# Performance work log

Measured on AMD Instinct MI355X. Metric: run time of the kernel, lower is better.

The kernel has to match this reference:

```python
import jax, jax.numpy as jnp
import numpy as np

N_NODES = 100000
N_EDGES = 1000000
N_GRAPHS = 64
NODE_IN = 4
HID = 64
SIG = 16
NEG_SLOPE = 0.2


def _gat_layer(x, src, dst, W, a_src, a_dst, bias, n_nodes, concat):
    # W: [H*D, F_in], a_src/a_dst: [H, D], bias: [H*D] or [D]
    H, D = a_src.shape
    h = (x @ W.T).reshape(-1, H, D)                      # [N, H, D]
    alpha_src = jnp.sum(h * a_src[None], axis=-1)        # [N, H]
    alpha_dst = jnp.sum(h * a_dst[None], axis=-1)        # [N, H]
    e = alpha_src[src] + alpha_dst[dst]                  # [E, H]
    e = jax.nn.leaky_relu(e, NEG_SLOPE)
    # segment softmax over edges grouped by destination node
    e_max = jax.ops.segment_max(e, dst, num_segments=n_nodes)   # [N, H]
    e_exp = jnp.exp(e - e_max[dst])                              # [E, H]
    denom = jax.ops.segment_sum(e_exp, dst, num_segments=n_nodes)
    alpha = e_exp / denom[dst]                                   # [E, H]
    out = jax.ops.segment_sum(alpha[:, :, None] * h[src], dst, num_segments=n_nodes)  # [N,H,D]
    if concat:
        out = out.reshape(-1, H * D)
    else:
        out = out.mean(axis=1)
    return out + bias


def setup_inputs() -> dict:
    key = jax.random.key(0)
    ks = jax.random.split(key, 16)
    x = jax.random.normal(ks[0], (N_NODES, NODE_IN), dtype=jnp.float32)
    edge_index = jax.random.randint(ks[1], (2, N_EDGES), 0, N_NODES, dtype=jnp.int32)
    batch = jnp.sort(jax.random.randint(ks[2], (N_NODES,), 0, N_GRAPHS, dtype=jnp.int32))
    s = 0.1
    # conv1: heads=2, concat -> out 128
    w1 = jax.random.normal(ks[3], (2 * HID, NODE_IN), dtype=jnp.float32) * s
    att_src1 = jax.random.normal(ks[4], (2, HID), dtype=jnp.float32) * s
    att_dst1 = jax.random.normal(ks[5], (2, HID), dtype=jnp.float32) * s
    b1 = jnp.zeros((2 * HID,), dtype=jnp.float32)
    # conv2: heads=1, mean -> out 64
    w2 = jax.random.normal(ks[6], (HID, 2 * HID), dtype=jnp.float32) * s
    att_src2 = jax.random.normal(ks[7], (1, HID), dtype=jnp.float32) * s
    att_dst2 = jax.random.normal(ks[8], (1, HID), dtype=jnp.float32) * s
    b2 = jnp.zeros((HID,), dtype=jnp.float32)
    wp = jax.random.normal(ks[9], (SIG, HID), dtype=jnp.float32) * s
    bp = jnp.zeros((SIG,), dtype=jnp.float32)
    return {"x": x, "edge_index": edge_index, "batch": batch,
            "w1": w1, "att_src1": att_src1, "att_dst1": att_dst1, "b1": b1,
            "w2": w2, "att_src2": att_src2, "att_dst2": att_dst2, "b2": b2,
            "wp": wp, "bp": bp}


def reference(x, edge_index, batch, w1, att_src1, att_dst1, b1,
              w2, att_src2, att_dst2, b2, wp, bp):
    n = x.shape[0]
    loops = jnp.arange(n, dtype=edge_index.dtype)
    src = jnp.concatenate([edge_index[0], loops])  # PyG GATConv adds self-loops
    dst = jnp.concatenate([edge_index[1], loops])
    h = jax.nn.elu(_gat_layer(x, src, dst, w1, att_src1, att_dst1, b1, n, concat=True))
    h = jax.nn.elu(_gat_layer(h, src, dst, w2, att_src2, att_dst2, b2, n, concat=False))
    # global mean pool by graph id
    sums = jax.ops.segment_sum(h, batch, num_segments=N_GRAPHS)
    cnts = jax.ops.segment_sum(jnp.ones((n,), h.dtype), batch, num_segments=N_GRAPHS)
    pooled = sums / jnp.maximum(cnts, 1.0)[:, None]
    return (pooled @ wp.T + bp).squeeze()
```

## Files before the change

kernel.cpp:

```cpp
#include <hip/hip_runtime.h>
#include <hip/hip_fp16.h>

#define N_NODES  100000
#define N_EDGES  1000000
#define E_TOT    1100000
#define E_CAP    1900000
#define N_GRAPHS 64

#define BSH    9
#define BSIZE  512
#define NBUCK  ((N_NODES + BSIZE - 1) / BSIZE)
#define CHUNK  4096
#define NBLKS  ((E_TOT + CHUNK - 1) / CHUNK)

typedef _Float16 half8 __attribute__((ext_vector_type(8)));
typedef float    f32x4 __attribute__((ext_vector_type(4)));

__device__ __forceinline__ float elu_f(float v) {
    return v > 0.f ? v : expm1f(v);
}

__device__ __forceinline__ float lrelu(float v) {
    return v > 0.f ? v : 0.2f * v;
}

__device__ __forceinline__ int lbound(const int* __restrict__ a, int n, int v) {
    int lo = 0, hi = n;
    while (lo < hi) { int m = (lo + hi) >> 1; if (a[m] < v) lo = m + 1; else hi = m; }
    return lo;
}

__global__ void k_preall(const float* __restrict__ w1,
                         const float* __restrict__ as1v, const float* __restrict__ ad1v,
                         const float* __restrict__ w2,
                         const float* __restrict__ as2v, const float* __restrict__ ad2v,
                         float* __restrict__ A1, float* __restrict__ D1,
                         float* __restrict__ B2, float* __restrict__ E2,
                         __half* __restrict__ w2frag,
                         int* __restrict__ bucketCount, float* __restrict__ pool,
                         const int* __restrict__ batch, float* __restrict__ cnt)
{
    if (blockIdx.x == 0) {
        int t = threadIdx.x;
        if (t < 128) {
            float acc = 0.f;
            for (int d = 0; d < 64; ++d) acc += w2[d * 128 + t] * as2v[d];
            B2[t] = acc;
        } else {
            int k = t - 128;
            float acc = 0.f;
            for (int d = 0; d < 64; ++d) acc += w2[d * 128 + k] * ad2v[d];
            E2[k] = acc;
        }
        if (t < 8) {
            int h = t >> 2, k = t & 3;
            float acc = 0.f;
            for (int d = 0; d < 64; ++d) acc += w1[(h * 64 + d) * 4 + k] * as1v[h * 64 + d];
            A1[t] = acc;
        } else if (t < 16) {
            int i = t - 8, h = i >> 2, k = i & 3;
            float acc = 0.f;
            for (int d = 0; d < 64; ++d) acc += w1[(h * 64 + d) * 4 + k] * ad1v[h * 64 + d];
            D1[i] = acc;
        }
        if (t < NBUCK) bucketCount[t] = 0;
        if (t < N_GRAPHS) {
            int a = lbound(batch, N_NODES, t);
            int b = lbound(batch, N_NODES, t + 1);
            cnt[t] = (float)(b - a);
        }
    } else {
        int f = (blockIdx.x - 1) * 256 + threadIdx.x;
        int j = f & 7, ln = (f >> 3) & 63, g = f >> 9;
        int nt = g >> 2, ks = g & 3;
        int col = nt * 16 + (ln & 15);
        int k   = ks * 32 + ((ln >> 4) << 3) + j;
        w2frag[f] = __float2half(w2[col * 128 + k]);
        if (f < N_GRAPHS * 64) pool[f] = 0.f;
    }
}

__global__ void __launch_bounds__(256) k_bin1(
    const int* __restrict__ ei, int* __restrict__ bucketCount, int* __restrict__ blockoff)
{
    __shared__ int hist[NBUCK];
    const int t = threadIdx.x;
    for (int i = t; i < NBUCK; i += 256) hist[i] = 0;
    __syncthreads();
    const int e0 = blockIdx.x * CHUNK;
    for (int i = t; i < CHUNK; i += 256) {
        int e = e0 + i;
        if (e < E_TOT) {
            int dst = (e < N_EDGES) ? ei[N_EDGES + e] : (e - N_EDGES);
            atomicAdd(&hist[dst >> BSH], 1);
        }
    }
    __syncthreads();
    for (int i = t; i < NBUCK; i += 256)
        blockoff[blockIdx.x * NBUCK + i] = atomicAdd(&bucketCount[i], hist[i]);
}

__global__ void __launch_bounds__(256) k_bin2(
    const int* __restrict__ ei, const int* __restrict__ bucketCount,
    const int* __restrict__ blockoff, int* __restrict__ bucketStart,
    unsigned int* __restrict__ bucketed)
{
    __shared__ int sh[256];
    __shared__ int cur[NBUCK];
    const int t = threadIdx.x;
    int v = (t < NBUCK) ? bucketCount[t] : 0;
    int acc = v;
    sh[t] = acc; __syncthreads();
    for (int off = 1; off < 256; off <<= 1) {
        int add = (t >= off) ? sh[t - off] : 0;
        __syncthreads();
        acc += add; sh[t] = acc; __syncthreads();
    }
    if (t < NBUCK) {
        int st = acc - v;
        cur[t] = st + blockoff[blockIdx.x * NBUCK + t];
        if (blockIdx.x == 0) bucketStart[t] = st;
    }
    __syncthreads();
    const int e0 = blockIdx.x * CHUNK;
    for (int i = t; i < CHUNK; i += 256) {
        int e = e0 + i;
        if (e < E_TOT) {
            int src = (e < N_EDGES) ? ei[e] : (e - N_EDGES);
            int dst = (e < N_EDGES) ? ei[N_EDGES + e] : (e - N_EDGES);
            int b = dst >> BSH;
            int p = atomicAdd(&cur[b], 1);
            bucketed[p] = (unsigned)src | ((unsigned)(dst & (BSIZE - 1)) << 17);
        }
    }
}

__global__ void __launch_bounds__(256) k_bhist(
    const unsigned int* __restrict__ bucketed,
    const int* __restrict__ bucketStart, const int* __restrict__ bucketCount,
    int* __restrict__ deg, int* __restrict__ rowptr, int* __restrict__ bucketPad)
{
    __shared__ int hist[BSIZE];
    __shared__ int sh[256];
    const int t = threadIdx.x;
    const int b = blockIdx.x;
    hist[t] = 0; hist[t + 256] = 0;
    __syncthreads();
    const int beg = bucketStart[b], cnt = bucketCount[b];
    for (int i = t; i < cnt; i += 256)
        atomicAdd(&hist[bucketed[beg + i] >> 17], 1);
    __syncthreads();
    int h0 = hist[2 * t], h1 = hist[2 * t + 1];
    int a = (h0 + 7) & ~7, c = (h1 + 7) & ~7;
    int s = a + c;
    sh[t] = s; __syncthreads();
    for (int off = 1; off < 256; off <<= 1) {
        int add = (t >= off) ? sh[t - off] : 0;
        __syncthreads();
        s += add; sh[t] = s; __syncthreads();
    }
    int base = s - a - c;
    const int n0 = b * BSIZE;
    int na = n0 + 2 * t, nb = n0 + 2 * t + 1;
    if (na < N_NODES) { deg[na] = h0; rowptr[na] = base; }
    if (nb < N_NODES) { deg[nb] = h1; rowptr[nb] = base + a; }
    if (t == 255) bucketPad[b] = s;
}

__global__ void __launch_bounds__(256) k_bscat(
    const unsigned int* __restrict__ bucketed,
    const int* __restrict__ bucketStart, const int* __restrict__ bucketCount,
    const int* __restrict__ bucketPad,
    int* __restrict__ rowptr, int* __restrict__ srcs)
{
    __shared__ int sh[256];
    __shared__ int excl[NBUCK];
    __shared__ int cur[BSIZE];
    const int t = threadIdx.x;
    const int b = blockIdx.x;

    int v = (t < NBUCK) ? bucketPad[t] : 0;
    int acc = v;
    sh[t] = acc; __syncthreads();
    for (int off = 1; off < 256; off <<= 1) {
        int add = (t >= off) ? sh[t - off] : 0;
        __syncthreads();
        acc += add; sh[t] = acc; __syncthreads();
    }
    if (t < NBUCK) excl[t] = acc - v;
    if (b == 0 && t == NBUCK - 1) rowptr[N_NODES] = acc;
    __syncthreads();
    const int base = excl[b];

    const int n0 = b * BSIZE;
    #pragma unroll
    for (int k = 0; k < 2; ++k) {
        int nl = t + k * 256;
        int n = n0 + nl;
        if (n < N_NODES) {
            int r = rowptr[n] + base;
            rowptr[n] = r;
            cur[nl] = r;
        }
    }
    __syncthreads();
    const int beg = bucketStart[b], cnt = bucketCount[b];
    for (int i = t; i < cnt; i += 256) {
        unsigned p = bucketed[beg + i];
        int rank = atomicAdd(&cur[p >> 17], 1);
        srcs[rank] = (int)(p & 0x1FFFFu);
    }
    __syncthreads();
    const int bend = base + bucketPad[b];
    #pragma unroll
    for (int k = 0; k < 2; ++k) {
        int nl = t + k * 256;
        int n = n0 + nl;
        if (n < N_NODES) {
            int e = (nl == BSIZE - 1 || n == N_NODES - 1) ? bend : rowptr[n + 1];
            for (int j = cur[nl]; j < e; ++j) srcs[j] = -1;
        }
    }
}

__global__ void __launch_bounds__(256) k_gather1x(
    const int* __restrict__ srcs, const int* __restrict__ rowptr, const int* __restrict__ deg,
    const float* __restrict__ x,
    const float* __restrict__ A1c, const float* __restrict__ D1c,
    float4* __restrict__ agg0, float4* __restrict__ agg1, float2* __restrict__ wsA)
{
    const int tid  = threadIdx.x;
    const int n    = blockIdx.x * 16 + (tid >> 4);
    const int lane = tid & 15;
    if (n >= N_NODES) return;

    const float4 A0 = ((const float4*)A1c)[0], A1v = ((const float4*)A1c)[1];
    const float4 D0 = ((const float4*)D1c)[0], D1v = ((const float4*)D1c)[1];
    const float4 xn = ((const float4*)x)[n];
    const float ad0 = xn.x * D0.x + xn.y * D0.y + xn.z * D0.z + xn.w * D0.w;
    const float ad1 = xn.x * D1v.x + xn.y * D1v.y + xn.z * D1v.z + xn.w * D1v.w;

    const int beg = rowptr[n], rend = beg + deg[n];
    float4 acc0 = {0.f, 0.f, 0.f, 0.f}, acc1 = {0.f, 0.f, 0.f, 0.f};
    float ws0 = 0.f, ws1 = 0.f;
    for (int j = beg + lane; j < rend; j += 16) {
        const int s = srcs[j];
        const float4 xs = ((const float4*)x)[s];
        const float as0 = xs.x * A0.x + xs.y * A0.y + xs.z * A0.z + xs.w * A0.w;
        const float as1 = xs.x * A1v.x + xs.y * A1v.y + xs.z * A1v.z + xs.w * A1v.w;
        const float w0 = __expf(lrelu(as0 + ad0));
        const float w1 = __expf(lrelu(as1 + ad1));
        acc0.x = fmaf(w0, xs.x, acc0.x); acc0.y = fmaf(w0, xs.y, acc0.y);
        acc0.z = fmaf(w0, xs.z, acc0.z); acc0.w = fmaf(w0, xs.w, acc0.w);
        acc1.x = fmaf(w1, xs.x, acc1.x); acc1.y = fmaf(w1, xs.y, acc1.y);
        acc1.z = fmaf(w1, xs.z, acc1.z); acc1.w = fmaf(w1, xs.w, acc1.w);
        ws0 += w0; ws1 += w1;
    }
    #pragma unroll
    for (int off = 1; off < 16; off <<= 1) {
        acc0.x += __shfl_xor(acc0.x, off, 64);
        acc0.y += __shfl_xor(acc0.y, off, 64);
        acc0.z += __shfl_xor(acc0.z, off, 64);
        acc0.w += __shfl_xor(acc0.w, off, 64);
        acc1.x += __shfl_xor(acc1.x, off, 64);
        acc1.y += __shfl_xor(acc1.y, off, 64);
        acc1.z += __shfl_xor(acc1.z, off, 64);
        acc1.w += __shfl_xor(acc1.w, off, 64);
        ws0    += __shfl_xor(ws0,    off, 64);
        ws1    += __shfl_xor(ws1,    off, 64);
    }
    if (lane == 0) {
        agg0[n] = acc0;
        agg1[n] = acc1;
        wsA[n]  = make_float2(ws0, ws1);
    }
}

#define H2_NPB 64
#define SROW_H_LD 136
__global__ void __launch_bounds__(256) k_h2f(
    const float4* __restrict__ agg0, const float4* __restrict__ agg1,
    const float2* __restrict__ wsA,
    const float* __restrict__ w1, const float* __restrict__ b1,
    const __half* __restrict__ w2frag,
    const float* __restrict__ B2, const float* __restrict__ E2,
    __half* __restrict__ h2h, float* __restrict__ as2, float* __restrict__ ad2)
{
    __shared__ __align__(16) _Float16 srow[H2_NPB * SROW_H_LD];
    const int tid = threadIdx.x;
    const int bn  = blockIdx.x * H2_NPB;

    #pragma unroll 4
    for (int t = 0; t < 16; ++t) {
        int i = tid + t * 256;
        int r = i >> 6, c2 = i & 63;
        int n = bn + r;
        int head = c2 >> 5;
        float4 a; float ws;
        if (n < N_NODES) {
            a = head ? agg1[n] : agg0[n];
            float2 w = wsA[n];
            ws = head ? w.y : w.x;
        } else { a = make_float4(0.f, 0.f, 0.f, 0.f); ws = 1.f; }
        const float4 wA = ((const float4*)w1)[2 * c2];
        const float4 wB = ((const float4*)w1)[2 * c2 + 1];
        const float2 bb = ((const float2*)b1)[c2];
        float inv = 1.f / ws;
        float v0 = elu_f((a.x * wA.x + a.y * wA.y + a.z * wA.z + a.w * wA.w) * inv + bb.x);
        float v1 = elu_f((a.x * wB.x + a.y * wB.y + a.z * wB.z + a.w * wB.w) * inv + bb.y);
        *(__half2*)&srow[r * SROW_H_LD + 2 * c2] = __floats2half2_rn(v0, v1);
    }
    __syncthreads();

    {
        int r = tid >> 2, q = tid & 3;
        const __half2* row = (const __half2*)&srow[r * SROW_H_LD];
        float ps = 0.f, pd = 0.f;
        #pragma unroll 4
        for (int i = 0; i < 16; ++i) {
            int c2 = q * 16 + i;
            float2 v  = __half22float2(row[c2]);
            float2 Bv = ((const float2*)B2)[c2];
            float2 Ev = ((const float2*)E2)[c2];
            ps += v.x * Bv.x + v.y * Bv.y;
            pd += v.x * Ev.x + v.y * Ev.y;
        }
        ps += __shfl_xor(ps, 1, 64); ps += __shfl_xor(ps, 2, 64);
        pd += __shfl_xor(pd, 1, 64); pd += __shfl_xor(pd, 2, 64);
        int n = bn + r;
        if (q == 0 && n < N_NODES) { as2[n] = ps; ad2[n] = pd; }
    }

    const int lane = tid & 63;
    const int wv   = tid >> 6;
    const int mrow = lane & 15;
    const int kc   = lane >> 4;
    f32x4 acc[4] = {{0.f,0.f,0.f,0.f},{0.f,0.f,0.f,0.f},{0.f,0.f,0.f,0.f},{0.f,0.f,0.f,0.f}};
    const half8* __restrict__ wf = (const half8*)w2frag;
    #pragma unroll
    for (int ks = 0; ks < 4; ++ks) {
        const half8 af = *(const half8*)&srow[(wv * 16 + mrow) * SROW_H_LD + ks * 32 + kc * 8];
        #pragma unroll
        for (int nt = 0; nt < 4; ++nt) {
            const half8 bf = wf[(nt * 4 + ks) * 64 + lane];
            acc[nt] = __builtin_amdgcn_mfma_f32_16x16x32_f16(af, bf, acc[nt], 0, 0, 0);
        }
    }
    #pragma unroll
    for (int nt = 0; nt < 4; ++nt) {
        #pragma unroll
        for (int reg = 0; reg < 4; ++reg) {
            int node = bn + wv * 16 + ((lane >> 4) << 2) + reg;
            int dim  = nt * 16 + (lane & 15);
            if (node < N_NODES) h2h[(size_t)node * 64 + dim] = __float2half(acc[nt][reg]);
        }
    }
}

__global__ void __launch_bounds__(256) k_gather2(
    const int* __restrict__ srcs, const int* __restrict__ rowptr,
    const float* __restrict__ as2, const float* __restrict__ ad2,
    const _Float16* __restrict__ h2h, const float* __restrict__ b2,
    __half* __restrict__ out2h)
{
    const int tid  = threadIdx.x;
    const int n    = blockIdx.x * 4 + (tid >> 6);
    const int lane = tid & 63;
    const int eg   = lane >> 3;
    const int dq   = lane & 7;
    const int beg = rowptr[n], end = rowptr[n + 1];
    const float adv = ad2[n];

    half8 hacc = {0, 0, 0, 0, 0, 0, 0, 0};
    float wsum = 0.f;
    for (int j = beg + eg; j < end; j += 8) {
        const int s = srcs[j];
        const int sa = (s >= 0) ? s : 0;
        float w = 0.f;
        if (s >= 0) w = __expf(lrelu(as2[s] + adv));
        const half8 v = *(const half8*)&h2h[(size_t)sa * 64 + dq * 8];
        const _Float16 wh = (_Float16)w;
        const half8 ws8 = {wh, wh, wh, wh, wh, wh, wh, wh};
        hacc += v * ws8;
        wsum += w;
    }
    float a0 = (float)hacc[0], a1 = (float)hacc[1], a2 = (float)hacc[2], a3 = (float)hacc[3];
    float a4 = (float)hacc[4], a5 = (float)hacc[5], a6 = (float)hacc[6], a7 = (float)hacc[7];
    #pragma unroll
    for (int off = 8; off < 64; off <<= 1) {
        a0 += __shfl_xor(a0, off, 64);
        a1 += __shfl_xor(a1, off, 64);
        a2 += __shfl_xor(a2, off, 64);
        a3 += __shfl_xor(a3, off, 64);
        a4 += __shfl_xor(a4, off, 64);
        a5 += __shfl_xor(a5, off, 64);
        a6 += __shfl_xor(a6, off, 64);
        a7 += __shfl_xor(a7, off, 64);
        wsum += __shfl_xor(wsum, off, 64);
    }
    if (eg == 0) {
        const float inv = 1.f / wsum;
        const float4 bA = ((const float4*)b2)[dq * 2];
        const float4 bB = ((const float4*)b2)[dq * 2 + 1];
        __half2 p0 = __floats2half2_rn(elu_f(a0 * inv + bA.x), elu_f(a1 * inv + bA.y));
        __half2 p1 = __floats2half2_rn(elu_f(a2 * inv + bA.z), elu_f(a3 * inv + bA.w));
        __half2 p2 = __floats2half2_rn(elu_f(a4 * inv + bB.x), elu_f(a5 * inv + bB.y));
        __half2 p3 = __floats2half2_rn(elu_f(a6 * inv + bB.z), elu_f(a7 * inv + bB.w));
        uint4 pk;
        pk.x = *(unsigned int*)&p0; pk.y = *(unsigned int*)&p1;
        pk.z = *(unsigned int*)&p2; pk.w = *(unsigned int*)&p3;
        *(uint4*)&out2h[(size_t)n * 64 + dq * 8] = pk;
    }
}

__global__ void __launch_bounds__(256) k_pool(
    const __half* __restrict__ out2h, const int* __restrict__ batch,
    float* __restrict__ pool)
{
    const int wv = threadIdx.x >> 6, d = threadIdx.x & 63;
    const int wid = blockIdx.x * 4 + wv;
    const int per = (N_NODES + 2047) / 2048;
    int n0 = wid * per, n1 = min(n0 + per, N_NODES);
    if (n0 >= n1) return;
    float acc = 0.f; int g = batch[n0];
    for (int n = n0; n < n1; ++n) {
        int gn = batch[n];
        if (gn != g) {
            atomicAdd(&pool[g * 64 + d], acc);
            acc = 0.f; g = gn;
        }
        acc += __half2float(out2h[(size_t)n * 64 + d]);
    }
    atomicAdd(&pool[g * 64 + d], acc);
}

__global__ void k_head(const float* __restrict__ pool, const float* __restrict__ cnt,
                       const float* __restrict__ wp, const float* __restrict__ bp,
                       float* __restrict__ out)
{
    int t = threadIdx.x;
    int g = t >> 4, s = t & 15;
    float c = cnt[g]; if (c < 1.f) c = 1.f;
    float acc = bp[s];
    for (int d = 0; d < 64; ++d) acc += (pool[g * 64 + d] / c) * wp[s * 64 + d];
    out[g * 16 + s] = acc;
}

extern "C" void kernel_launch(void* const* d_in, const int* in_sizes, int n_in,
                              void* d_out, int out_size, void* d_ws, size_t ws_size,
                              hipStream_t stream)
{
    const float* x     = (const float*)d_in[0];
    const int*   ei    = (const int*)  d_in[1];
    const int*   batch = (const int*)  d_in[2];
    const float* w1    = (const float*)d_in[3];
    const float* asr1  = (const float*)d_in[4];
    const float* adr1  = (const float*)d_in[5];
    const float* b1    = (const float*)d_in[6];
    const float* w2    = (const float*)d_in[7];
    const float* asr2  = (const float*)d_in[8];
    const float* adr2  = (const float*)d_in[9];
    const float* b2    = (const float*)d_in[10];
    const float* wp    = (const float*)d_in[11];
    const float* bp    = (const float*)d_in[12];
    float* out = (float*)d_out;

    float4* agg0 = (float4*)d_ws;
    float4* agg1 = agg0 + N_NODES;
    float2* wsA  = (float2*)(agg1 + N_NODES);
    __half* h2h  = (__half*)(wsA + N_NODES);
    __half* out2h = h2h + (size_t)N_NODES * 64;
    float* as2   = (float*)(out2h + (size_t)N_NODES * 64);
    float* ad2   = as2 + N_NODES;
    float* pool  = ad2 + N_NODES;
    float* cnt   = pool + N_GRAPHS * 64;
    int* deg     = (int*)(cnt + N_GRAPHS);
    int* rowptr  = deg + N_NODES;
    unsigned int* bucketed = (unsigned int*)(rowptr + N_NODES + 1);
    int* srcs    = (int*)(bucketed + E_TOT);
    int* blockoff    = srcs + E_CAP;
    int* bucketCount = blockoff + NBLKS * NBUCK;
    int* bucketStart = bucketCount + NBUCK;
    int* bucketPad   = bucketStart + NBUCK;
    float* A1    = (float*)(bucketPad + NBUCK);
    float* D1    = A1 + 8;
    float* B2    = D1 + 8;
    float* E2    = B2 + 128;
    __half* w2frag = (__half*)(((uintptr_t)(E2 + 128) + 15) & ~(uintptr_t)15);

    k_preall<<<33, 256, 0, stream>>>(w1, asr1, adr1, w2, asr2, adr2,
                                     A1, D1, B2, E2, w2frag, bucketCount, pool,
                                     batch, cnt);

    k_bin1 <<<NBLKS, 256, 0, stream>>>(ei, bucketCount, blockoff);
    k_bin2 <<<NBLKS, 256, 0, stream>>>(ei, bucketCount, blockoff, bucketStart, bucketed);
    k_bhist<<<NBUCK, 256, 0, stream>>>(bucketed, bucketStart, bucketCount, deg, rowptr, bucketPad);
    k_bscat<<<NBUCK, 256, 0, stream>>>(bucketed, bucketStart, bucketCount, bucketPad,
                                       rowptr, srcs);

    const int gb = (N_NODES + 15) / 16;
    k_gather1x<<<gb, 256, 0, stream>>>(srcs, rowptr, deg, x, A1, D1, agg0, agg1, wsA);

    k_h2f<<<(N_NODES + H2_NPB - 1) / H2_NPB, 256, 0, stream>>>(
        agg0, agg1, wsA, w1, b1, w2frag, B2, E2, h2h, as2, ad2);

    k_gather2<<<N_NODES / 4, 256, 0, stream>>>(srcs, rowptr, as2, ad2,
                                               (const _Float16*)h2h, b2, out2h);

    k_pool<<<512, 256, 0, stream>>>(out2h, batch, pool);
    k_head<<<1, 1024, 0, stream>>>(pool, cnt, wp, bp, out);
}
```

Before: 195.6 us.

## Fuse bucket histogram and scatter into one CSR kernel with slack-padded offsets

Merges the per-bucket histogram and scatter kernels into a single kernel. Each bucket's CSR base is taken from its bucket start plus a fixed per-bucket slack, so the global scan over padded bucket sizes is no longer needed. Bucket entries are staged in LDS when they fit, which avoids reading them from global memory twice. The end of each row is now computed from deg instead of rowptr[n+1], which requires srcs to have room for the slack and leaves gaps between buckets.

Result: no change. 192.6 us (-1.5%).

```diff
diff --git a/kernel.cpp b/kernel.cpp
--- a/kernel.cpp
+++ b/kernel.cpp
@@ -12,6 +12,8 @@
 #define NBUCK  ((N_NODES + BSIZE - 1) / BSIZE)
 #define CHUNK  4096
 #define NBLKS  ((E_TOT + CHUNK - 1) / CHUNK)
+#define BSLACK (7 * BSIZE)
+#define EBUF   8192
 
 typedef _Float16 half8 __attribute__((ext_vector_type(8)));
 typedef float    f32x4 __attribute__((ext_vector_type(4)));
@@ -135,21 +137,35 @@
     }
 }
 
-__global__ void __launch_bounds__(256) k_bhist(
+__global__ void __launch_bounds__(256) k_bcsr(
     const unsigned int* __restrict__ bucketed,
     const int* __restrict__ bucketStart, const int* __restrict__ bucketCount,
-    int* __restrict__ deg, int* __restrict__ rowptr, int* __restrict__ bucketPad)
+    int* __restrict__ deg, int* __restrict__ rowptr, int* __restrict__ srcs)
 {
     __shared__ int hist[BSIZE];
     __shared__ int sh[256];
+    __shared__ int cur[BSIZE];
+    __shared__ unsigned ebuf[EBUF];
     const int t = threadIdx.x;
     const int b = blockIdx.x;
+    const int beg = bucketStart[b], cnt = bucketCount[b];
+    const int base = beg + BSLACK * b;
+    const bool lds = (cnt <= EBUF);
+
     hist[t] = 0; hist[t + 256] = 0;
     __syncthreads();
-    const int beg = bucketStart[b], cnt = bucketCount[b];
-    for (int i = t; i < cnt; i += 256)
-        atomicAdd(&hist[bucketed[beg + i] >> 17], 1);
-    __syncthreads();
+    if (lds) {
+        for (int i = t; i < cnt; i += 256) {
+            unsigned p = bucketed[beg + i];
+            ebuf[i] = p;
+            atomicAdd(&hist[p >> 17], 1);
+        }
+    } else {
+        for (int i = t; i < cnt; i += 256)
+            atomicAdd(&hist[bucketed[beg + i] >> 17], 1);
+    }
+    __syncthreads();
+
     int h0 = hist[2 * t], h1 = hist[2 * t + 1];
     int a = (h0 + 7) & ~7, c = (h1 + 7) & ~7;
     int s = a + c;
@@ -159,65 +175,27 @@
         __syncthreads();
         s += add; sh[t] = s; __syncthreads();
     }
-    int base = s - a - c;
+    int lb = s - a - c;
     const int n0 = b * BSIZE;
     int na = n0 + 2 * t, nb = n0 + 2 * t + 1;
-    if (na < N_NODES) { deg[na] = h0; rowptr[na] = base; }
-    if (nb < N_NODES) { deg[nb] = h1; rowptr[nb] = base + a; }
-    if (t == 255) bucketPad[b] = s;
-}
-
-__global__ void __launch_bounds__(256) k_bscat(
-    const unsigned int* __restrict__ bucketed,
-    const int* __restrict__ bucketStart, const int* __restrict__ bucketCount,
-    const int* __restrict__ bucketPad,
-    int* __restrict__ rowptr, int* __restrict__ srcs)
-{
-    __shared__ int sh[256];
-    __shared__ int excl[NBUCK];
-    __shared__ int cur[BSIZE];
-    const int t = threadIdx.x;
-    const int b = blockIdx.x;
-
-    int v = (t < NBUCK) ? bucketPad[t] : 0;
-    int acc = v;
-    sh[t] = acc; __syncthreads();
-    for (int off = 1; off < 256; off <<= 1) {
-        int add = (t >= off) ? sh[t - off] : 0;
-        __syncthreads();
-        acc += add; sh[t] = acc; __syncthreads();
-    }
-    if (t < NBUCK) excl[t] = acc - v;
-    if (b == 0 && t == NBUCK - 1) rowptr[N_NODES] = acc;
-    __syncthreads();
-    const int base = excl[b];
-
-    const int n0 = b * BSIZE;
+    if (na < N_NODES) { deg[na] = h0; rowptr[na] = base + lb;     cur[2 * t]     = base + lb; }
+    if (nb < N_NODES) { deg[nb] = h1; rowptr[nb] = base + lb + a; cur[2 * t + 1] = base + lb + a; }
+    __syncthreads();
+
+    for (int i = t; i < cnt; i += 256) {
+        unsigned p = lds ? ebuf[i] : bucketed[beg + i];
+        int rank = atomicAdd(&cur[p >> 17], 1);
+        srcs[rank] = (int)(p & 0x1FFFFu);
+    }
+    __syncthreads();
+
     #pragma unroll
     for (int k = 0; k < 2; ++k) {
         int nl = t + k * 256;
         int n = n0 + nl;
         if (n < N_NODES) {
-            int r = rowptr[n] + base;
-            rowptr[n] = r;
-            cur[nl] = r;
-        }
-    }
-    __syncthreads();
-    const int beg = bucketStart[b], cnt = bucketCount[b];
-    for (int i = t; i < cnt; i += 256) {
-        unsigned p = bucketed[beg + i];
-        int rank = atomicAdd(&cur[p >> 17], 1);
-        srcs[rank] = (int)(p & 0x1FFFFu);
-    }
-    __syncthreads();
-    const int bend = base + bucketPad[b];
-    #pragma unroll
-    for (int k = 0; k < 2; ++k) {
-        int nl = t + k * 256;
-        int n = n0 + nl;
-        if (n < N_NODES) {
-            int e = (nl == BSIZE - 1 || n == N_NODES - 1) ? bend : rowptr[n + 1];
+            int d  = (nl & 1) ? hist[nl] : hist[nl];
+            int e  = cur[nl] + (((d + 7) & ~7) - d);
             for (int j = cur[nl]; j < e; ++j) srcs[j] = -1;
         }
     }
@@ -358,7 +336,7 @@
 }
 
 __global__ void __launch_bounds__(256) k_gather2(
-    const int* __restrict__ srcs, const int* __restrict__ rowptr,
+    const int* __restrict__ srcs, const int* __restrict__ rowptr, const int* __restrict__ deg,
     const float* __restrict__ as2, const float* __restrict__ ad2,
     const _Float16* __restrict__ h2h, const float* __restrict__ b2,
     __half* __restrict__ out2h)
@@ -368,7 +346,8 @@
     const int lane = tid & 63;
     const int eg   = lane >> 3;
     const int dq   = lane & 7;
-    const int beg = rowptr[n], end = rowptr[n + 1];
+    const int beg = rowptr[n];
+    const int end = beg + ((deg[n] + 7) & ~7);
     const float adv = ad2[n];
 
     half8 hacc = {0, 0, 0, 0, 0, 0, 0, 0};
@@ -476,13 +455,12 @@
     float* cnt   = pool + N_GRAPHS * 64;
     int* deg     = (int*)(cnt + N_GRAPHS);
     int* rowptr  = deg + N_NODES;
-    unsigned int* bucketed = (unsigned int*)(rowptr + N_NODES + 1);
+    unsigned int* bucketed = (unsigned int*)(rowptr + N_NODES);
     int* srcs    = (int*)(bucketed + E_TOT);
     int* blockoff    = srcs + E_CAP;
     int* bucketCount = blockoff + NBLKS * NBUCK;
     int* bucketStart = bucketCount + NBUCK;
-    int* bucketPad   = bucketStart + NBUCK;
-    float* A1    = (float*)(bucketPad + NBUCK);
+    float* A1    = (float*)(bucketStart + NBUCK);
     float* D1    = A1 + 8;
     float* B2    = D1 + 8;
     float* E2    = B2 + 128;
@@ -492,11 +470,9 @@
                                      A1, D1, B2, E2, w2frag, bucketCount, pool,
                                      batch, cnt);
 
-    k_bin1 <<<NBLKS, 256, 0, stream>>>(ei, bucketCount, blockoff);
-    k_bin2 <<<NBLKS, 256, 0, stream>>>(ei, bucketCount, blockoff, bucketStart, bucketed);
-    k_bhist<<<NBUCK, 256, 0, stream>>>(bucketed, bucketStart, bucketCount, deg, rowptr, bucketPad);
-    k_bscat<<<NBUCK, 256, 0, stream>>>(bucketed, bucketStart, bucketCount, bucketPad,
-                                       rowptr, srcs);
+    k_bin1<<<NBLKS, 256, 0, stream>>>(ei, bucketCount, blockoff);
+    k_bin2<<<NBLKS, 256, 0, stream>>>(ei, bucketCount, blockoff, bucketStart, bucketed);
+    k_bcsr<<<NBUCK, 256, 0, stream>>>(bucketed, bucketStart, bucketCount, deg, rowptr, srcs);
 
     const int gb = (N_NODES + 15) / 16;
     k_gather1x<<<gb, 256, 0, stream>>>(srcs, rowptr, deg, x, A1, D1, agg0, agg1, wsA);
@@ -504,7 +480,7 @@
     k_h2f<<<(N_NODES + H2_NPB - 1) / H2_NPB, 256, 0, stream>>>(
         agg0, agg1, wsA, w1, b1, w2frag, B2, E2, h2h, as2, ad2);
 
-    k_gather2<<<N_NODES / 4, 256, 0, stream>>>(srcs, rowptr, as2, ad2,
+    k_gather2<<<N_NODES / 4, 256, 0, stream>>>(srcs, rowptr, deg, as2, ad2,
                                                (const _Float16*)h2h, b2, out2h);
 
     k_pool<<<512, 256, 0, stream>>>(out2h, batch, pool);
```
